# Optimization experiments

Hardware: AMD Instinct MI355X
Metric: run time of the kernel (lower is better)

The kernel has to match this reference:

```python
import jax, jax.numpy as jnp
import numpy as np

B, S, DIM, NQ, NKV = 2, 2048, 4096, 32, 8
HD = DIM // NQ  # 128


def _rope(t, fc):
    # t: [B,S,H,D]; fc: [S,D/2,2] = (cos,sin). Complex multiply on (even,odd) pairs.
    b, s, h, d = t.shape
    tp = t.astype(jnp.float32).reshape(b, s, h, d // 2, 2)
    c = fc[None, :, None, :, 0]
    sn = fc[None, :, None, :, 1]
    x0, x1 = tp[..., 0], tp[..., 1]
    rot = jnp.stack([x0 * c - x1 * sn, x0 * sn + x1 * c], axis=-1)
    return rot.reshape(b, s, h, d).astype(t.dtype)


def setup_inputs() -> dict:
    key = jax.random.key(0)
    ks = jax.random.split(key, 5)
    x = jax.random.normal(ks[0], (B, S, DIM), jnp.float32)
    wq = jax.random.normal(ks[1], (DIM, NQ * HD), jnp.float32) * 0.02
    wk = jax.random.normal(ks[2], (DIM, NKV * HD), jnp.float32) * 0.02
    wv = jax.random.normal(ks[3], (DIM, NKV * HD), jnp.float32) * 0.02
    wo = jax.random.normal(ks[4], (NQ * HD, DIM), jnp.float32) * 0.02
    # Llama RoPE frequencies for positions [0, S)
    inv_freq = 1.0 / (10000.0 ** (jnp.arange(0, HD, 2, dtype=jnp.float32) / HD))
    ang = jnp.arange(S, dtype=jnp.float32)[:, None] * inv_freq[None, :]  # [S, HD/2]
    freqs_cis = jnp.stack([jnp.cos(ang), jnp.sin(ang)], axis=-1)  # [S, HD/2, 2]
    cache_key = jnp.zeros((B, S, NKV, HD), jnp.float32)
    cache_value = jnp.zeros((B, S, NKV, HD), jnp.float32)
    return {"x": x, "start_pos": 0, "freqs_cis": freqs_cis, "wq": wq, "wk": wk,
            "wv": wv, "wo": wo, "cache_key": cache_key, "cache_value": cache_value}


def reference(x, start_pos, freqs_cis, wq, wk, wv, wo, cache_key, cache_value):
    b, s, dim = x.shape
    nkv, hd = cache_key.shape[2], cache_key.shape[3]
    nq = wq.shape[1] // hd
    n_rep = nq // nkv
    xq = (x @ wq).reshape(b, s, nq, hd)
    xk = (x @ wk).reshape(b, s, nkv, hd)
    xv = (x @ wv).reshape(b, s, nkv, hd)
    xq = _rope(xq, freqs_cis)
    xk = _rope(xk, freqs_cis)
    # KV-cache write then read of the valid prefix
    ck = jax.lax.dynamic_update_slice(cache_key, xk, (0, start_pos, 0, 0))
    cv = jax.lax.dynamic_update_slice(cache_value, xv, (0, start_pos, 0, 0))
    kv_len = start_pos + s
    k = ck[:, :kv_len]
    v = cv[:, :kv_len]
    # GQA: repeat_interleave kv heads to match q heads (as original materializes)
    keys = jnp.repeat(k, n_rep, axis=2)    # [B,K,NQ,HD]
    values = jnp.repeat(v, n_rep, axis=2)
    scale = 1.0 / jnp.sqrt(jnp.float32(hd))
    scores = jnp.einsum('bqhd,bkhd->bhqk', xq, keys) * scale  # [B,H,S,K]
    attn = jax.nn.softmax(scores, axis=-1)  # NOTE: no causal mask, as in source
    out = jnp.einsum('bhqk,bkhd->bqhd', attn, values).reshape(b, s, nq * hd)
    return out @ wo
```

## Files before the change

kernel.cpp:

```cpp
#include <hip/hip_runtime.h>
#include <stdint.h>


typedef __attribute__((ext_vector_type(8))) short short8;
typedef __attribute__((ext_vector_type(4))) float f32x4;
typedef __attribute__((ext_vector_type(16))) float f32x16;

#define DEVFN static __device__ __forceinline__

DEVFN ushort f2bf(float f) {
  uint32_t u = __builtin_bit_cast(uint32_t, f);
  u += 0x7fffu + ((u >> 16) & 1);
  return (ushort)(u >> 16);
}

DEVFN void gll16(const void* g, void* l) {
  __builtin_amdgcn_global_load_lds(
      (const __attribute__((address_space(1))) void*)g,
      (__attribute__((address_space(3))) void*)l, 16, 0, 0);
}

DEVFN float xhalf_max(float v) { return fmaxf(v, __shfl_xor(v, 32)); }
DEVFN float xhalf_add(float v) { return v + __shfl_xor(v, 32); }

#if __has_builtin(__builtin_amdgcn_exp2f)
DEVFN float ex2(float x) { return __builtin_amdgcn_exp2f(x); }
#else
DEVFN float ex2(float x) {
  float r;
  asm("v_exp_f32 %0, %1" : "=v"(r) : "v"(x));
  return r;
}
#endif

DEVFN uint32_t cvtpk(float a, float b) {
  uint32_t r;
  asm("v_cvt_pk_bf16_f32 %0, %1, %2" : "=v"(r) : "v"(a), "v"(b));
  return r;
}

DEVFN float vmax16(const f32x16& v) {
  float a0 = fmaxf(fmaxf(v[0], v[1]), v[2]);
  float a1 = fmaxf(fmaxf(v[3], v[4]), v[5]);
  float a2 = fmaxf(fmaxf(v[6], v[7]), v[8]);
  float a3 = fmaxf(fmaxf(v[9], v[10]), v[11]);
  float a4 = fmaxf(fmaxf(v[12], v[13]), v[14]);
  float b0 = fmaxf(fmaxf(a0, a1), a2);
  float b1 = fmaxf(fmaxf(a3, a4), v[15]);
  return fmaxf(b0, b1);
}
DEVFN float vsum16(const f32x16& v) {
  float s0 = (v[0] + v[1]) + (v[2] + v[3]);
  float s1 = (v[4] + v[5]) + (v[6] + v[7]);
  float s2 = (v[8] + v[9]) + (v[10] + v[11]);
  float s3 = (v[12] + v[13]) + (v[14] + v[15]);
  return (s0 + s1) + (s2 + s3);
}

DEVFN short8 mk_frag(uint32_t w0, uint32_t w1, uint32_t w2, uint32_t w3, int hi) {
  uint32_t x0 = __shfl_xor(w0, 32);
  uint32_t x1 = __shfl_xor(w1, 32);
  uint32_t x2 = __shfl_xor(w2, 32);
  uint32_t x3 = __shfl_xor(w3, 32);
  uint4 u;
  u.x = hi ? x2 : w0;
  u.y = hi ? x3 : w1;
  u.z = hi ? w2 : x0;
  u.w = hi ? w3 : x1;
  return __builtin_bit_cast(short8, u);
}

#define VMW(N) asm volatile("s_waitcnt vmcnt(" #N ")" ::: "memory")

__global__ __launch_bounds__(256) void k_cvt(const float* __restrict__ src,
                                             ushort* __restrict__ dst, int n8) {
  int i = blockIdx.x * 256 + threadIdx.x;
  if (i >= n8) return;
  const float4* s4 = (const float4*)src + (size_t)i * 2;
  float4 a = s4[0], b = s4[1];
  uint4 o;
  o.x = (uint32_t)f2bf(a.x) | ((uint32_t)f2bf(a.y) << 16);
  o.y = (uint32_t)f2bf(a.z) | ((uint32_t)f2bf(a.w) << 16);
  o.z = (uint32_t)f2bf(b.x) | ((uint32_t)f2bf(b.y) << 16);
  o.w = (uint32_t)f2bf(b.z) | ((uint32_t)f2bf(b.w) << 16);
  ((uint4*)dst)[i] = o;
}

__global__ __launch_bounds__(256) void k_tr(const float* __restrict__ src,
                                            ushort* __restrict__ dst, int R, int C) {
  __shared__ ushort tl[64 * 64];
  const int c0 = blockIdx.x * 64, r0 = blockIdx.y * 64;
  const int t = threadIdx.x;
  const int r = t >> 4, c4 = (t & 15) << 2;
#pragma unroll
  for (int i = 0; i < 4; ++i) {
    const int rr = r + i * 16;
    float4 v = *(const float4*)&src[(size_t)(r0 + rr) * C + c0 + c4];
    ushort bv[4] = {f2bf(v.x), f2bf(v.y), f2bf(v.z), f2bf(v.w)};
#pragma unroll
    for (int j = 0; j < 4; ++j) {
      const int c = c4 + j;
      *(ushort*)((char*)tl + c * 128 + (((rr >> 3) ^ (c & 7)) << 4) +
                 ((rr & 7) << 1)) = bv[j];
    }
  }
  __syncthreads();
  const int cc = t >> 2;
#pragma unroll
  for (int i = 0; i < 2; ++i) {
    const int ch = (t & 3) + i * 4;
    short8 v = *(const short8*)((char*)tl + cc * 128 + ((ch ^ (cc & 7)) << 4));
    *(short8*)&dst[(size_t)(c0 + cc) * R + r0 + ch * 8] = v;
  }
}

template <int MODE>
__global__ __launch_bounds__(512, 2) void k_gemm8(
    const ushort* __restrict__ A, const ushort* __restrict__ Bp,
    const float* __restrict__ fcis, ushort* __restrict__ oQ,
    ushort* __restrict__ oK, ushort* __restrict__ oV, float* __restrict__ oC) {
  constexpr int K = 4096;
  constexpr int BN = MODE ? 256 : 192;
  constexpr int NBX = MODE ? 16 : 32;
  constexpr int ABUF = 16384;
  constexpr int BBUF = BN * 64;
  constexpr int NT = K / 32;
  constexpr int WNG = MODE ? 4 : 2;
  constexpr int MF = MODE ? 8 : 4;
  constexpr int NF = MODE ? 4 : 6;
  constexpr int MH = MF / 2;
  constexpr int MSPAN = 16 * MF;
  constexpr int NSPAN = 16 * NF;

  __shared__ char smem[4 * ABUF + 4 * BBUF];
  char* AsL = smem;
  char* BsL = smem + 4 * ABUF;

  constexpr int nwg = NBX * 16;
  const int bid = blockIdx.x;
  const int wg = (bid & 7) * (nwg >> 3) + (bid >> 3);
  const int nb = wg % NBX, mb = wg / NBX;
  const int m0 = mb * 256, n0 = nb * BN;

  const int tid = threadIdx.x;
  const int w = tid >> 6, lane = tid & 63;
  const int gg = lane >> 4, rr = lane & 15;
  const int wm = w / WNG, wn = w % WNG;

  const int l8 = lane >> 3, s7 = lane & 7;
  const int Ra0 = w * 8 + l8, Ra1 = 64 + Ra0;
  const int ea0 = s7 ^ (Ra0 & 7), ea1 = s7 ^ (Ra1 & 7);
  const ushort* agp0 = A + (size_t)(m0 + 2 * Ra0 + (ea0 >> 2)) * K + (ea0 & 3) * 8;
  const ushort* agp1 = A + (size_t)(m0 + 2 * Ra1 + (ea1 >> 2)) * K + (ea1 & 3) * 8;
  char* lda0 = AsL + w * 1024;
  char* lda1 = AsL + 8192 + w * 1024;

  const int Rb0 = w * 8 + l8;
  const int eb0 = s7 ^ (Rb0 & 7);
  const ushort* bgp0 = Bp + (size_t)(n0 + 2 * Rb0 + (eb0 >> 2)) * K + (eb0 & 3) * 8;
  char* ldb0 = BsL + w * 1024;
  const int Rb1 = MODE ? (64 + w * 8 + l8) : (64 + w * 4 + l8);
  const int eb1 = s7 ^ (Rb1 & 7);
  const ushort* bgp1 = Bp + (size_t)(n0 + 2 * Rb1 + (eb1 >> 2)) * K + (eb1 & 3) * 8;
  char* ldb1 = BsL + 8192 + (MODE ? w * 1024 : w * 512);

  auto STAGE_A = [&](int t) {
    const int bo = t & 3;
    const size_t ko = (size_t)t * 32;
    gll16(agp0 + ko, lda0 + bo * ABUF);
    gll16(agp1 + ko, lda1 + bo * ABUF);
  };
  auto STAGE_B = [&](int t) {
    const int bo = t & 3;
    const size_t ko = (size_t)t * 32;
    gll16(bgp0 + ko, ldb0 + bo * BBUF);
    if constexpr (MODE) {
      gll16(bgp1 + ko, ldb1 + bo * BBUF);
    } else {
      if (lane < 32) gll16(bgp1 + ko, ldb1 + bo * BBUF);
    }
  };

  int aoff[MF], boff[NF];
#pragma unroll
  for (int mf = 0; mf < MF; ++mf) {
    const int m = wm * MSPAN + mf * 16 + rr;
    aoff[mf] = (m >> 1) * 128 + (((((m & 1) << 2) | gg) ^ ((m >> 1) & 7)) << 4);
  }
#pragma unroll
  for (int nf = 0; nf < NF; ++nf) {
    const int n = wn * NSPAN + nf * 16 + rr;
    boff[nf] = (n >> 1) * 128 + (((((n & 1) << 2) | gg) ^ ((n >> 1) & 7)) << 4);
  }

  f32x4 acc[MF][NF] = {};
  short8 X0[MH], X1[MH], Y0[MH], Y1[MH];
  short8 Bc0[NF], Bc1[NF];

  auto RD_A = [&](int tt, short8* d, int h) {
    const char* Ab = AsL + (tt & 3) * ABUF;
#pragma unroll
    for (int i = 0; i < MH; ++i) d[i] = *(const short8*)(Ab + aoff[h * MH + i]);
  };
  auto RD_B = [&](int tt, short8* d) {
    const char* Bb = BsL + (tt & 3) * BBUF;
#pragma unroll
    for (int nf = 0; nf < NF; ++nf) d[nf] = *(const short8*)(Bb + boff[nf]);
  };
  auto MFMA_H = [&](short8* a, short8* bfr, int h) {
#pragma unroll
    for (int mi = 0; mi < MH; ++mi)
#pragma unroll
      for (int nf = 0; nf < NF; ++nf)
        acc[h + mi][nf] = __builtin_amdgcn_mfma_f32_16x16x32_bf16(
            a[mi], bfr[nf], acc[h + mi][nf], 0, 0, 0);
  };

#define GITER(T, cA0, cA1, cB, nA0, nA1, nB, STG, VN)                \
  do {                                                               \
    if constexpr (MODE == 1) RD_B((T), Bc0); \
    RD_A((T) + 1, nA0, 0);                                           \
    if constexpr (MODE == 0) RD_B((T) + 1, nB);                      \
    __builtin_amdgcn_sched_barrier(0);                               \
    __builtin_amdgcn_s_setprio(1);                                   \
    MFMA_H(cA0, (MODE == 1) ? Bc0 : cB, 0);                          \
    __builtin_amdgcn_s_setprio(0);                                   \
    RD_A((T) + 1, nA1, 1);                                           \
    if (STG) { STAGE_A((T) + 3); STAGE_B((T) + 3); }                 \
    __builtin_amdgcn_sched_barrier(0);                               \
    __builtin_amdgcn_s_setprio(1);                                   \
    MFMA_H(cA1, (MODE == 1) ? Bc0 : cB, MH);                         \
    __builtin_amdgcn_s_setprio(0);                                   \
    VMW(VN);                                                         \
    __builtin_amdgcn_s_barrier();                                    \
    __builtin_amdgcn_sched_barrier(0);                               \
  } while (0)

  STAGE_A(0); STAGE_B(0);
  STAGE_A(1); STAGE_B(1);
  STAGE_A(2); STAGE_B(2);
  VMW(4);
  __builtin_amdgcn_s_barrier();
  __builtin_amdgcn_sched_barrier(0);
  RD_A(0, X0, 0);
  RD_A(0, X1, 1);
  if constexpr (MODE == 0) RD_B(0, Bc0);

  for (int tp = 0; tp < 62; ++tp) {
    const int T = 2 * tp;
    GITER(T, X0, X1, Bc0, Y0, Y1, Bc1, true, 4);
    GITER(T + 1, Y0, Y1, Bc1, X0, X1, Bc0, true, 4);
  }
  GITER(124, X0, X1, Bc0, Y0, Y1, Bc1, true, 4);
  GITER(125, Y0, Y1, Bc1, X0, X1, Bc0, false, 0);
  GITER(126, X0, X1, Bc0, Y0, Y1, Bc1, false, 0);
  if constexpr (MODE == 1) RD_B(127, Bc0);
  __builtin_amdgcn_s_setprio(1);
  MFMA_H(Y0, (MODE == 1) ? Bc0 : Bc1, 0);
  MFMA_H(Y1, (MODE == 1) ? Bc0 : Bc1, MH);
  __builtin_amdgcn_s_setprio(0);
#undef GITER

  if constexpr (MODE == 1) {
#pragma unroll
    for (int mf = 0; mf < MF; ++mf) {
      const int mbase = m0 + wm * MSPAN + mf * 16 + gg * 4;
#pragma unroll
      for (int nf = 0; nf < NF; ++nf) {
        const int n = n0 + wn * NSPAN + nf * 16 + rr;
#pragma unroll
        for (int j = 0; j < 4; ++j)
          oC[(size_t)(mbase + j) * 4096 + n] = acc[mf][nf][j];
      }
    }
  } else {
    const int b = m0 >> 11;
#pragma unroll
    for (int mf = 0; mf < MF; ++mf) {
      const int mbase = m0 + wm * MSPAN + mf * 16 + gg * 4;
      const int s0 = mbase & 2047;
#pragma unroll
      for (int nf = 0; nf < NF; ++nf) {
        const int n = n0 + wn * NSPAN + nf * 16 + rr;
        if (n < 5120) {
          const int d = n & 127, ii = d >> 1;
          const float sgn = (n & 1) ? 1.0f : -1.0f;
          const float qsc = (n < 4096) ? 0.12752364599362f : 1.0f;
          ushort res[4];
#pragma unroll
          for (int j = 0; j < 4; ++j) {
            const float2 cs = ((const float2*)fcis)[(size_t)(s0 + j) * 64 + ii];
            float v = acc[mf][nf][j];
            float pv = __shfl_xor(v, 1);
            res[j] = f2bf(qsc * (v * cs.x + sgn * pv * cs.y));
          }
          if (n < 4096) {
            ushort* dst = oQ + ((size_t)(b * 32 + (n >> 7)) * 2048 + s0) * 128 + d;
#pragma unroll
            for (int j = 0; j < 4; ++j) dst[j * 128] = res[j];
          } else {
            ushort* dst =
                oK + ((size_t)(b * 8 + ((n - 4096) >> 7)) * 2048 + s0) * 128 + d;
#pragma unroll
            for (int j = 0; j < 4; ++j) dst[j * 128] = res[j];
          }
        } else {
          const int n2 = n - 5120;
          ushort4 pk;
          pk.x = f2bf(acc[mf][nf][0]);
          pk.y = f2bf(acc[mf][nf][1]);
          pk.z = f2bf(acc[mf][nf][2]);
          pk.w = f2bf(acc[mf][nf][3]);
          *(ushort4*)&oV[((size_t)(b * 8 + (n2 >> 7)) * 128 + (n2 & 127)) * 2048 + s0] =
              pk;
        }
      }
    }
  }
}

__global__ __launch_bounds__(512, 2) void k_attn(const ushort* __restrict__ Qg,
                                                 const ushort* __restrict__ Kg,
                                                 const ushort* __restrict__ Vt,
                                                 ushort* __restrict__ Og) {
  __shared__ ushort Ks[2][64 * 128];
  __shared__ ushort Vs[2][64 * 128];
  __shared__ float sml[8][32];

  const int bh = blockIdx.x, qt = blockIdx.y;
  const int b = bh >> 5, h = bh & 31, hk = h >> 2;
  const int t = threadIdx.x, w = t >> 6, lane = t & 63;
  const int ln31 = lane & 31, hi = lane >> 5;
  const int q0 = qt * 256;

  short8 qf[8];
  {
    const size_t qbase = ((size_t)bh * 2048 + q0 + w * 32 + ln31) * 128;
#pragma unroll
    for (int tt = 0; tt < 8; ++tt)
      qf[tt] = *(const short8*)&Qg[qbase + tt * 16 + hi * 8];
  }
  const size_t kgb = (size_t)(b * 8 + hk) * 2048 * 128;
  const size_t vgb = (size_t)(b * 8 + hk) * 128 * 2048;

  const int srow = t >> 3;
  const int ssl = (t & 7) * 2;
  const int s0 = ssl ^ (srow & 15);
  const int vd = 2 * (t >> 3) + ((t & 7) >> 2);
  const int vkl = (t & 3) * 16;
  const ushort* kgp = Kg + kgb + (size_t)srow * 128 + ssl * 8;
  const ushort* vgp = Vt + vgb + (size_t)vd * 2048 + vkl;

  uint4 rk0, rk1, rv0, rv1;
  auto LOAD = [&](int k0) {
    const uint4* kp = (const uint4*)(kgp + (size_t)k0 * 128);
    rk0 = kp[0];
    rk1 = kp[1];
    const uint4* vp = (const uint4*)(vgp + k0);
    rv0 = vp[0];
    rv1 = vp[1];
  };
  auto STORE = [&](int buf) {
    char* kd = (char*)Ks[buf] + srow * 256;
    *(uint4*)(kd + (s0 << 4)) = rk0;
    *(uint4*)(kd + ((s0 ^ 1) << 4)) = rk1;
    char* vdd = (char*)Vs[buf] + srow * 256;
    *(uint4*)(vdd + (s0 << 4)) = rv0;
    *(uint4*)(vdd + ((s0 ^ 1) << 4)) = rv1;
  };

  f32x16 ov[4] = {};
  float m_run = -1e30f, l_run = 0.f;

  const int mk = ln31 & 15;
  const int krb0 = ln31 * 256, krb1 = krb0 + 8192;
  const int vrb = (ln31 >> 1) * 256;
  const int vsp = (ln31 & 1) * 8 + hi;
  const int mv = ln31 >> 1;

  LOAD(0);
  STORE(0);
  __syncthreads();

  for (int tile = 0; tile < 32; ++tile) {
    const int cur = tile & 1;
    if (tile < 31) LOAD((tile + 1) * 64);

    const char* Kc = (const char*)Ks[cur];
    f32x16 p0 = {}, p1 = {};
    __builtin_amdgcn_s_setprio(1);
#pragma unroll
    for (int tt = 0; tt < 8; ++tt) {
      const int sl = ((tt * 2 + hi) ^ mk) << 4;
      short8 ka0 = *(const short8*)(Kc + krb0 + sl);
      short8 ka1 = *(const short8*)(Kc + krb1 + sl);
      p0 = __builtin_amdgcn_mfma_f32_32x32x16_bf16(ka0, qf[tt], p0, 0, 0, 0);
      p1 = __builtin_amdgcn_mfma_f32_32x32x16_bf16(ka1, qf[tt], p1, 0, 0, 0);
    }
    __builtin_amdgcn_s_setprio(0);

    const float pmax = xhalf_max(fmaxf(vmax16(p0), vmax16(p1)));
    if (!__all(pmax <= m_run + 8.0f)) {
      const float mnew = fmaxf(m_run, pmax);
      const float al = ex2(m_run - mnew);
      m_run = mnew;
      l_run *= al;
      sml[w][ln31] = al;
      const float4 a0 = *(const float4*)&sml[w][hi * 4];
      const float4 a1 = *(const float4*)&sml[w][8 + hi * 4];
      const float4 a2 = *(const float4*)&sml[w][16 + hi * 4];
      const float4 a3 = *(const float4*)&sml[w][24 + hi * 4];
      const float aa[16] = {a0.x, a0.y, a0.z, a0.w, a1.x, a1.y, a1.z, a1.w,
                            a2.x, a2.y, a2.z, a2.w, a3.x, a3.y, a3.z, a3.w};
#pragma unroll
      for (int i = 0; i < 16; ++i) {
        ov[0][i] *= aa[i]; ov[1][i] *= aa[i];
        ov[2][i] *= aa[i]; ov[3][i] *= aa[i];
      }
    }
#pragma unroll
    for (int i = 0; i < 16; ++i) p0[i] = ex2(p0[i] - m_run);
#pragma unroll
    for (int i = 0; i < 16; ++i) p1[i] = ex2(p1[i] - m_run);
    l_run += xhalf_add(vsum16(p0) + vsum16(p1));

    short8 pa[4];
    pa[0] = mk_frag(cvtpk(p0[0], p0[1]), cvtpk(p0[2], p0[3]),
                    cvtpk(p0[4], p0[5]), cvtpk(p0[6], p0[7]), hi);
    pa[1] = mk_frag(cvtpk(p0[8], p0[9]), cvtpk(p0[10], p0[11]),
                    cvtpk(p0[12], p0[13]), cvtpk(p0[14], p0[15]), hi);
    pa[2] = mk_frag(cvtpk(p1[0], p1[1]), cvtpk(p1[2], p1[3]),
                    cvtpk(p1[4], p1[5]), cvtpk(p1[6], p1[7]), hi);
    pa[3] = mk_frag(cvtpk(p1[8], p1[9]), cvtpk(p1[10], p1[11]),
                    cvtpk(p1[12], p1[13]), cvtpk(p1[14], p1[15]), hi);

    const char* Vc = (const char*)Vs[cur];
    __builtin_amdgcn_s_setprio(1);
#pragma unroll
    for (int db = 0; db < 4; ++db) {
      const int rb = vrb + db * 4096;
#pragma unroll
      for (int ks = 0; ks < 4; ++ks) {
        const int sl = ((vsp + ks * 2) ^ mv) << 4;
        short8 bv = *(const short8*)(Vc + rb + sl);
        ov[db] = __builtin_amdgcn_mfma_f32_32x32x16_bf16(pa[ks], bv, ov[db], 0, 0, 0);
      }
    }
    __builtin_amdgcn_s_setprio(0);

    if (tile < 31) STORE(cur ^ 1);
    __syncthreads();
  }

  sml[w][ln31] = l_run;
  const float4 l0 = *(const float4*)&sml[w][hi * 4];
  const float4 l1 = *(const float4*)&sml[w][8 + hi * 4];
  const float4 l2 = *(const float4*)&sml[w][16 + hi * 4];
  const float4 l3 = *(const float4*)&sml[w][24 + hi * 4];
  const float inv[16] = {1.f / l0.x, 1.f / l0.y, 1.f / l0.z, 1.f / l0.w,
                         1.f / l1.x, 1.f / l1.y, 1.f / l1.z, 1.f / l1.w,
                         1.f / l2.x, 1.f / l2.y, 1.f / l2.z, 1.f / l2.w,
                         1.f / l3.x, 1.f / l3.y, 1.f / l3.z, 1.f / l3.w};
  const int qb0 = q0 + w * 32 + hi * 4;
#pragma unroll
  for (int rg = 0; rg < 4; ++rg)
#pragma unroll
    for (int j = 0; j < 4; ++j) {
      const int sq = qb0 + rg * 8 + j;
      const size_t orow = ((size_t)(b * 2048 + sq)) * 4096 + h * 128 + ln31;
#pragma unroll
      for (int db = 0; db < 4; ++db)
        Og[orow + db * 32] = f2bf(ov[db][rg * 4 + j] * inv[rg * 4 + j]);
    }
}

extern "C" void kernel_launch(void* const* d_in, const int* in_sizes, int n_in,
                              void* d_out, int out_size, void* d_ws, size_t ws_size,
                              hipStream_t stream) {
  const float* x = (const float*)d_in[0];
  const float* fcis = (const float*)d_in[2];
  const float* wq = (const float*)d_in[3];
  const float* wk = (const float*)d_in[4];
  const float* wv = (const float*)d_in[5];
  const float* wo = (const float*)d_in[6];
  float* out = (float*)d_out;

  char* ws = (char*)d_ws;
  ushort* xb  = (ushort*)(ws);
  ushort* wsT = (ushort*)(ws + 33554432u);
  ushort* qb  = (ushort*)(ws + 83886080u);
  ushort* kb  = (ushort*)(ws + 117440512u);
  ushort* vbT = (ushort*)(ws + 125829120u);
  ushort* woT = xb;
  ushort* ao  = wsT;

  k_cvt<<<8192, 256, 0, stream>>>(x, xb, 2097152);
  k_tr<<<dim3(64, 64), 256, 0, stream>>>(wq, wsT, 4096, 4096);
  k_tr<<<dim3(16, 64), 256, 0, stream>>>(wk, wsT + (size_t)4096 * 4096, 4096, 1024);
  k_tr<<<dim3(16, 64), 256, 0, stream>>>(wv, wsT + (size_t)5120 * 4096, 4096, 1024);
  k_gemm8<0><<<512, 512, 0, stream>>>(xb, wsT, fcis, qb, kb, vbT, nullptr);
  k_tr<<<dim3(64, 64), 256, 0, stream>>>(wo, woT, 4096, 4096);
  k_attn<<<dim3(64, 8), 512, 0, stream>>>(qb, kb, vbT, ao);
  k_gemm8<1><<<256, 512, 0, stream>>>(ao, woT, nullptr, nullptr, nullptr, nullptr,
                                      out);
}
```

Measured before the change: 527.7 us.

## Deepen GEMM LDS ring to five stages and barrier every other iteration

The bf16 GEMM's LDS staging ring grows from four to five buffers, with prefetch distance raised from three to four k-tiles. Buffer offsets are tracked with rotating indices instead of `t & 3`. The workgroup barrier plus waits now run only every second k-iteration, and an explicit lgkmcnt(0) is added before each barrier. The goal is more latency hiding and fewer barrier stalls. The cost is about 160 KB of LDS, the full per-CU budget, and a risk of read/write races on buffers reused between barriers.

```diff
diff --git a/kernel.cpp b/kernel.cpp
--- a/kernel.cpp
+++ b/kernel.cpp
@@ -71,6 +71,7 @@
 }
 
 #define VMW(N) asm volatile("s_waitcnt vmcnt(" #N ")" ::: "memory")
+#define LGKM0 asm volatile("s_waitcnt lgkmcnt(0)" ::: "memory")
 
 __global__ __launch_bounds__(256) void k_cvt(const float* __restrict__ src,
                                              ushort* __restrict__ dst, int n8) {
@@ -132,9 +133,9 @@
   constexpr int MSPAN = 16 * MF;
   constexpr int NSPAN = 16 * NF;
 
-  __shared__ char smem[4 * ABUF + 4 * BBUF];
+  __shared__ char smem[5 * ABUF + 5 * BBUF];
   char* AsL = smem;
-  char* BsL = smem + 4 * ABUF;
+  char* BsL = smem + 5 * ABUF;
 
   constexpr int nwg = NBX * 16;
   const int bid = blockIdx.x;
@@ -164,20 +165,18 @@
   const ushort* bgp1 = Bp + (size_t)(n0 + 2 * Rb1 + (eb1 >> 2)) * K + (eb1 & 3) * 8;
   char* ldb1 = BsL + 8192 + (MODE ? w * 1024 : w * 512);
 
-  auto STAGE_A = [&](int t) {
-    const int bo = t & 3;
+  auto STAGE_A = [&](int t, int oo) {
     const size_t ko = (size_t)t * 32;
-    gll16(agp0 + ko, lda0 + bo * ABUF);
-    gll16(agp1 + ko, lda1 + bo * ABUF);
-  };
-  auto STAGE_B = [&](int t) {
-    const int bo = t & 3;
+    gll16(agp0 + ko, lda0 + oo);
+    gll16(agp1 + ko, lda1 + oo);
+  };
+  auto STAGE_B = [&](int t, int oo) {
     const size_t ko = (size_t)t * 32;
-    gll16(bgp0 + ko, ldb0 + bo * BBUF);
+    gll16(bgp0 + ko, ldb0 + oo);
     if constexpr (MODE) {
-      gll16(bgp1 + ko, ldb1 + bo * BBUF);
+      gll16(bgp1 + ko, ldb1 + oo);
     } else {
-      if (lane < 32) gll16(bgp1 + ko, ldb1 + bo * BBUF);
+      if (lane < 32) gll16(bgp1 + ko, ldb1 + oo);
     }
   };
 
@@ -197,13 +196,13 @@
   short8 X0[MH], X1[MH], Y0[MH], Y1[MH];
   short8 Bc0[NF], Bc1[NF];
 
-  auto RD_A = [&](int tt, short8* d, int h) {
-    const char* Ab = AsL + (tt & 3) * ABUF;
+  auto RD_A = [&](int oo, short8* d, int h) {
+    const char* Ab = AsL + oo;
 #pragma unroll
     for (int i = 0; i < MH; ++i) d[i] = *(const short8*)(Ab + aoff[h * MH + i]);
   };
-  auto RD_B = [&](int tt, short8* d) {
-    const char* Bb = BsL + (tt & 3) * BBUF;
+  auto RD_B = [&](int oo, short8* d) {
+    const char* Bb = BsL + oo;
 #pragma unroll
     for (int nf = 0; nf < NF; ++nf) d[nf] = *(const short8*)(Bb + boff[nf]);
   };
@@ -216,45 +215,60 @@
             a[mi], bfr[nf], acc[h + mi][nf], 0, 0, 0);
   };
 
-#define GITER(T, cA0, cA1, cB, nA0, nA1, nB, STG, VN)                \
-  do {                                                               \
-    if constexpr (MODE == 1) RD_B((T), Bc0); \
-    RD_A((T) + 1, nA0, 0);                                           \
-    if constexpr (MODE == 0) RD_B((T) + 1, nB);                      \
-    __builtin_amdgcn_sched_barrier(0);                               \
-    __builtin_amdgcn_s_setprio(1);                                   \
-    MFMA_H(cA0, (MODE == 1) ? Bc0 : cB, 0);                          \
-    __builtin_amdgcn_s_setprio(0);                                   \
-    RD_A((T) + 1, nA1, 1);                                           \
-    if (STG) { STAGE_A((T) + 3); STAGE_B((T) + 3); }                 \
-    __builtin_amdgcn_sched_barrier(0);                               \
-    __builtin_amdgcn_s_setprio(1);                                   \
-    MFMA_H(cA1, (MODE == 1) ? Bc0 : cB, MH);                         \
-    __builtin_amdgcn_s_setprio(0);                                   \
-    VMW(VN);                                                         \
-    __builtin_amdgcn_s_barrier();                                    \
-    __builtin_amdgcn_sched_barrier(0);                               \
+  int oA = 0, oB = 0;
+#define NXTA(o) ((o) + ABUF == 5 * ABUF ? 0 : (o) + ABUF)
+#define NXTB(o) ((o) + BBUF == 5 * BBUF ? 0 : (o) + BBUF)
+#define PRVA(o) ((o) == 0 ? 4 * ABUF : (o)-ABUF)
+#define PRVB(o) ((o) == 0 ? 4 * BBUF : (o)-BBUF)
+
+#define GITER(T, cA0, cA1, cB, nA0, nA1, nB, STG, BARM, VN)           \
+  do {                                                                \
+    const int nAo = NXTA(oA), nBo = NXTB(oB);                         \
+    if constexpr (MODE == 1) RD_B(oB, Bc0);  \
+    RD_A(nAo, nA0, 0);                                                \
+    if constexpr (MODE == 0) RD_B(nBo, nB);                           \
+    __builtin_amdgcn_sched_barrier(0);                                \
+    __builtin_amdgcn_s_setprio(1);                                    \
+    MFMA_H(cA0, (MODE == 1) ? Bc0 : cB, 0);                           \
+    __builtin_amdgcn_s_setprio(0);                                    \
+    RD_A(nAo, nA1, 1);                                                \
+    if (STG) { STAGE_A((T) + 4, PRVA(oA)); STAGE_B((T) + 4, PRVB(oB)); } \
+    __builtin_amdgcn_sched_barrier(0);                                \
+    __builtin_amdgcn_s_setprio(1);                                    \
+    MFMA_H(cA1, (MODE == 1) ? Bc0 : cB, MH);                          \
+    __builtin_amdgcn_s_setprio(0);                                    \
+    if (BARM) {                                                       \
+      LGKM0;                                                          \
+      VMW(VN);                                                        \
+      __builtin_amdgcn_s_barrier();                                   \
+      __builtin_amdgcn_sched_barrier(0);                              \
+    }                                                                 \
+    oA = nAo; oB = nBo;                                               \
   } while (0)
 
-  STAGE_A(0); STAGE_B(0);
-  STAGE_A(1); STAGE_B(1);
-  STAGE_A(2); STAGE_B(2);
+  STAGE_A(0, 0); STAGE_B(0, 0);
+  STAGE_A(1, ABUF); STAGE_B(1, BBUF);
+  STAGE_A(2, 2 * ABUF); STAGE_B(2, 2 * BBUF);
+  STAGE_A(3, 3 * ABUF); STAGE_B(3, 3 * BBUF);
   VMW(4);
   __builtin_amdgcn_s_barrier();
   __builtin_amdgcn_sched_barrier(0);
   RD_A(0, X0, 0);
   RD_A(0, X1, 1);
   if constexpr (MODE == 0) RD_B(0, Bc0);
+  LGKM0;
+  __builtin_amdgcn_s_barrier();
+  __builtin_amdgcn_sched_barrier(0);
 
   for (int tp = 0; tp < 62; ++tp) {
     const int T = 2 * tp;
-    GITER(T, X0, X1, Bc0, Y0, Y1, Bc1, true, 4);
-    GITER(T + 1, Y0, Y1, Bc1, X0, X1, Bc0, true, 4);
-  }
-  GITER(124, X0, X1, Bc0, Y0, Y1, Bc1, true, 4);
-  GITER(125, Y0, Y1, Bc1, X0, X1, Bc0, false, 0);
-  GITER(126, X0, X1, Bc0, Y0, Y1, Bc1, false, 0);
-  if constexpr (MODE == 1) RD_B(127, Bc0);
+    GITER(T, X0, X1, Bc0, Y0, Y1, Bc1, true, 0, 4);
+    GITER(T + 1, Y0, Y1, Bc1, X0, X1, Bc0, true, 1, 4);
+  }
+  GITER(124, X0, X1, Bc0, Y0, Y1, Bc1, false, 0, 4);
+  GITER(125, Y0, Y1, Bc1, X0, X1, Bc0, false, 1, 0);
+  GITER(126, X0, X1, Bc0, Y0, Y1, Bc1, false, 0, 4);
+  if constexpr (MODE == 1) RD_B(oB, Bc0);
   __builtin_amdgcn_s_setprio(1);
   MFMA_H(Y0, (MODE == 1) ? Bc0 : Bc1, 0);
   MFMA_H(Y1, (MODE == 1) ? Bc0 : Bc1, MH);
```

New measurement: 530.5 us. Within noise of the previous version (+0.5%).

## Restructure attention kernel: 64 query rows per wave, triple-buffered direct-to-LDS KV loads

Applied to the files above, without the earlier changes.

Each wave in the attention kernel now handles two 32-row query blocks that share each K and V fragment read from LDS. This halves LDS traffic per MFMA and doubles the query tile per block to 512, which also halves the grid. KV tiles shrink to 32 keys and are streamed with global_load_lds into a three-slot ring. This replaces the register round-trip and store-to-LDS double buffer and allows one barrier per tile. The costs are more accumulator registers, half as many blocks, and twice as many loop iterations.

```diff
diff --git a/kernel.cpp b/kernel.cpp
--- a/kernel.cpp
+++ b/kernel.cpp
@@ -218,7 +218,7 @@
 
 #define GITER(T, cA0, cA1, cB, nA0, nA1, nB, STG, VN)                \
   do {                                                               \
-    if constexpr (MODE == 1) RD_B((T), Bc0); \
+    if constexpr (MODE == 1) RD_B((T), Bc0);                         \
     RD_A((T) + 1, nA0, 0);                                           \
     if constexpr (MODE == 0) RD_B((T) + 1, nB);                      \
     __builtin_amdgcn_sched_barrier(0);                               \
@@ -323,155 +323,179 @@
                                                  const ushort* __restrict__ Kg,
                                                  const ushort* __restrict__ Vt,
                                                  ushort* __restrict__ Og) {
-  __shared__ ushort Ks[2][64 * 128];
-  __shared__ ushort Vs[2][64 * 128];
+  __shared__ ushort Ks[3 * 4096];
+  __shared__ ushort Vs[3 * 4096];
   __shared__ float sml[8][32];
 
   const int bh = blockIdx.x, qt = blockIdx.y;
   const int b = bh >> 5, h = bh & 31, hk = h >> 2;
   const int t = threadIdx.x, w = t >> 6, lane = t & 63;
   const int ln31 = lane & 31, hi = lane >> 5;
-  const int q0 = qt * 256;
-
-  short8 qf[8];
+  const int q0 = qt * 512;
+
+  short8 qfA[8], qfB[8];
   {
-    const size_t qbase = ((size_t)bh * 2048 + q0 + w * 32 + ln31) * 128;
-#pragma unroll
-    for (int tt = 0; tt < 8; ++tt)
-      qf[tt] = *(const short8*)&Qg[qbase + tt * 16 + hi * 8];
-  }
+    const size_t qbase = ((size_t)bh * 2048 + q0 + w * 64 + ln31) * 128;
+#pragma unroll
+    for (int tt = 0; tt < 8; ++tt) {
+      qfA[tt] = *(const short8*)&Qg[qbase + tt * 16 + hi * 8];
+      qfB[tt] = *(const short8*)&Qg[qbase + 32 * 128 + tt * 16 + hi * 8];
+    }
+  }
+
+  const int srow = w * 4 + (lane >> 4);
+  const int ssl = lane & 15;
   const size_t kgb = (size_t)(b * 8 + hk) * 2048 * 128;
   const size_t vgb = (size_t)(b * 8 + hk) * 128 * 2048;
-
-  const int srow = t >> 3;
-  const int ssl = (t & 7) * 2;
-  const int s0 = ssl ^ (srow & 15);
-  const int vd = 2 * (t >> 3) + ((t & 7) >> 2);
-  const int vkl = (t & 3) * 16;
-  const ushort* kgp = Kg + kgb + (size_t)srow * 128 + ssl * 8;
-  const ushort* vgp = Vt + vgb + (size_t)vd * 2048 + vkl;
-
-  uint4 rk0, rk1, rv0, rv1;
-  auto LOAD = [&](int k0) {
-    const uint4* kp = (const uint4*)(kgp + (size_t)k0 * 128);
-    rk0 = kp[0];
-    rk1 = kp[1];
-    const uint4* vp = (const uint4*)(vgp + k0);
-    rv0 = vp[0];
-    rv1 = vp[1];
+  const ushort* kgp = Kg + kgb + (size_t)srow * 128 + ((ssl ^ (srow & 15)) << 3);
+  const int vsi = ssl ^ (srow & 15);
+  const ushort* vgp =
+      Vt + vgb + (size_t)(srow * 4 + (vsi >> 2)) * 2048 + (vsi & 3) * 8;
+  char* kld = (char*)Ks + w * 1024;
+  char* vld = (char*)Vs + w * 1024;
+
+  auto STAGE = [&](int tt) {
+    const int sl = tt - (tt / 3) * 3;
+    gll16(kgp + (size_t)tt * 4096, kld + sl * 8192);
+    gll16(vgp + (size_t)tt * 32, vld + sl * 8192);
   };
-  auto STORE = [&](int buf) {
-    char* kd = (char*)Ks[buf] + srow * 256;
-    *(uint4*)(kd + (s0 << 4)) = rk0;
-    *(uint4*)(kd + ((s0 ^ 1) << 4)) = rk1;
-    char* vdd = (char*)Vs[buf] + srow * 256;
-    *(uint4*)(vdd + (s0 << 4)) = rv0;
-    *(uint4*)(vdd + ((s0 ^ 1) << 4)) = rv1;
-  };
-
-  f32x16 ov[4] = {};
-  float m_run = -1e30f, l_run = 0.f;
+
+  f32x16 ovA[4] = {}, ovB[4] = {};
+  float mA = -1e30f, lA = 0.f, mB = -1e30f, lB = 0.f;
 
   const int mk = ln31 & 15;
-  const int krb0 = ln31 * 256, krb1 = krb0 + 8192;
-  const int vrb = (ln31 >> 1) * 256;
-  const int vsp = (ln31 & 1) * 8 + hi;
-  const int mv = ln31 >> 1;
-
-  LOAD(0);
-  STORE(0);
+  const int krb = ln31 * 256;
+  const int vr0 = ln31 >> 2;
+  const int vsp = (ln31 & 3) * 4 + hi;
+
+  STAGE(0);
+  STAGE(1);
+  VMW(2);
   __syncthreads();
 
-  for (int tile = 0; tile < 32; ++tile) {
-    const int cur = tile & 1;
-    if (tile < 31) LOAD((tile + 1) * 64);
-
-    const char* Kc = (const char*)Ks[cur];
-    f32x16 p0 = {}, p1 = {};
+  for (int tile = 0; tile < 64; ++tile) {
+    const int sl = tile - (tile / 3) * 3;
+    if (tile < 62) STAGE(tile + 2);
+
+    const char* Kc = (const char*)Ks + sl * 8192;
+    f32x16 pA = {}, pB = {};
     __builtin_amdgcn_s_setprio(1);
 #pragma unroll
     for (int tt = 0; tt < 8; ++tt) {
-      const int sl = ((tt * 2 + hi) ^ mk) << 4;
-      short8 ka0 = *(const short8*)(Kc + krb0 + sl);
-      short8 ka1 = *(const short8*)(Kc + krb1 + sl);
-      p0 = __builtin_amdgcn_mfma_f32_32x32x16_bf16(ka0, qf[tt], p0, 0, 0, 0);
-      p1 = __builtin_amdgcn_mfma_f32_32x32x16_bf16(ka1, qf[tt], p1, 0, 0, 0);
+      short8 ka = *(const short8*)(Kc + krb + (((tt * 2 + hi) ^ mk) << 4));
+      pA = __builtin_amdgcn_mfma_f32_32x32x16_bf16(ka, qfA[tt], pA, 0, 0, 0);
+      pB = __builtin_amdgcn_mfma_f32_32x32x16_bf16(ka, qfB[tt], pB, 0, 0, 0);
     }
     __builtin_amdgcn_s_setprio(0);
 
-    const float pmax = xhalf_max(fmaxf(vmax16(p0), vmax16(p1)));
-    if (!__all(pmax <= m_run + 8.0f)) {
-      const float mnew = fmaxf(m_run, pmax);
-      const float al = ex2(m_run - mnew);
-      m_run = mnew;
-      l_run *= al;
-      sml[w][ln31] = al;
-      const float4 a0 = *(const float4*)&sml[w][hi * 4];
-      const float4 a1 = *(const float4*)&sml[w][8 + hi * 4];
-      const float4 a2 = *(const float4*)&sml[w][16 + hi * 4];
-      const float4 a3 = *(const float4*)&sml[w][24 + hi * 4];
-      const float aa[16] = {a0.x, a0.y, a0.z, a0.w, a1.x, a1.y, a1.z, a1.w,
-                            a2.x, a2.y, a2.z, a2.w, a3.x, a3.y, a3.z, a3.w};
-#pragma unroll
-      for (int i = 0; i < 16; ++i) {
-        ov[0][i] *= aa[i]; ov[1][i] *= aa[i];
-        ov[2][i] *= aa[i]; ov[3][i] *= aa[i];
+    short8 paA0, paA1, paB0, paB1;
+    {
+      const float pmax = xhalf_max(vmax16(pA));
+      if (!__all(pmax <= mA + 8.0f)) {
+        const float mnew = fmaxf(mA, pmax);
+        const float al = ex2(mA - mnew);
+        mA = mnew;
+        lA *= al;
+        sml[w][ln31] = al;
+        const float4 a0 = *(const float4*)&sml[w][hi * 4];
+        const float4 a1 = *(const float4*)&sml[w][8 + hi * 4];
+        const float4 a2 = *(const float4*)&sml[w][16 + hi * 4];
+        const float4 a3 = *(const float4*)&sml[w][24 + hi * 4];
+        const float aa[16] = {a0.x, a0.y, a0.z, a0.w, a1.x, a1.y, a1.z, a1.w,
+                              a2.x, a2.y, a2.z, a2.w, a3.x, a3.y, a3.z, a3.w};
+#pragma unroll
+        for (int i = 0; i < 16; ++i) {
+          ovA[0][i] *= aa[i]; ovA[1][i] *= aa[i];
+          ovA[2][i] *= aa[i]; ovA[3][i] *= aa[i];
+        }
       }
-    }
-#pragma unroll
-    for (int i = 0; i < 16; ++i) p0[i] = ex2(p0[i] - m_run);
-#pragma unroll
-    for (int i = 0; i < 16; ++i) p1[i] = ex2(p1[i] - m_run);
-    l_run += xhalf_add(vsum16(p0) + vsum16(p1));
-
-    short8 pa[4];
-    pa[0] = mk_frag(cvtpk(p0[0], p0[1]), cvtpk(p0[2], p0[3]),
-                    cvtpk(p0[4], p0[5]), cvtpk(p0[6], p0[7]), hi);
-    pa[1] = mk_frag(cvtpk(p0[8], p0[9]), cvtpk(p0[10], p0[11]),
-                    cvtpk(p0[12], p0[13]), cvtpk(p0[14], p0[15]), hi);
-    pa[2] = mk_frag(cvtpk(p1[0], p1[1]), cvtpk(p1[2], p1[3]),
-                    cvtpk(p1[4], p1[5]), cvtpk(p1[6], p1[7]), hi);
-    pa[3] = mk_frag(cvtpk(p1[8], p1[9]), cvtpk(p1[10], p1[11]),
-                    cvtpk(p1[12], p1[13]), cvtpk(p1[14], p1[15]), hi);
-
-    const char* Vc = (const char*)Vs[cur];
+#pragma unroll
+      for (int i = 0; i < 16; ++i) pA[i] = ex2(pA[i] - mA);
+      lA += xhalf_add(vsum16(pA));
+      paA0 = mk_frag(cvtpk(pA[0], pA[1]), cvtpk(pA[2], pA[3]),
+                     cvtpk(pA[4], pA[5]), cvtpk(pA[6], pA[7]), hi);
+      paA1 = mk_frag(cvtpk(pA[8], pA[9]), cvtpk(pA[10], pA[11]),
+                     cvtpk(pA[12], pA[13]), cvtpk(pA[14], pA[15]), hi);
+    }
+    {
+      const float pmax = xhalf_max(vmax16(pB));
+      if (!__all(pmax <= mB + 8.0f)) {
+        const float mnew = fmaxf(mB, pmax);
+        const float al = ex2(mB - mnew);
+        mB = mnew;
+        lB *= al;
+        sml[w][ln31] = al;
+        const float4 a0 = *(const float4*)&sml[w][hi * 4];
+        const float4 a1 = *(const float4*)&sml[w][8 + hi * 4];
+        const float4 a2 = *(const float4*)&sml[w][16 + hi * 4];
+        const float4 a3 = *(const float4*)&sml[w][24 + hi * 4];
+        const float aa[16] = {a0.x, a0.y, a0.z, a0.w, a1.x, a1.y, a1.z, a1.w,
+                              a2.x, a2.y, a2.z, a2.w, a3.x, a3.y, a3.z, a3.w};
+#pragma unroll
+        for (int i = 0; i < 16; ++i) {
+          ovB[0][i] *= aa[i]; ovB[1][i] *= aa[i];
+          ovB[2][i] *= aa[i]; ovB[3][i] *= aa[i];
+        }
+      }
+#pragma unroll
+      for (int i = 0; i < 16; ++i) pB[i] = ex2(pB[i] - mB);
+      lB += xhalf_add(vsum16(pB));
+      paB0 = mk_frag(cvtpk(pB[0], pB[1]), cvtpk(pB[2], pB[3]),
+                     cvtpk(pB[4], pB[5]), cvtpk(pB[6], pB[7]), hi);
+      paB1 = mk_frag(cvtpk(pB[8], pB[9]), cvtpk(pB[10], pB[11]),
+                     cvtpk(pB[12], pB[13]), cvtpk(pB[14], pB[15]), hi);
+    }
+
+    const char* Vc = (const char*)Vs + sl * 8192;
     __builtin_amdgcn_s_setprio(1);
 #pragma unroll
     for (int db = 0; db < 4; ++db) {
-      const int rb = vrb + db * 4096;
-#pragma unroll
-      for (int ks = 0; ks < 4; ++ks) {
-        const int sl = ((vsp + ks * 2) ^ mv) << 4;
-        short8 bv = *(const short8*)(Vc + rb + sl);
-        ov[db] = __builtin_amdgcn_mfma_f32_32x32x16_bf16(pa[ks], bv, ov[db], 0, 0, 0);
+      const int row = db * 8 + vr0;
+      const int rb = row * 256;
+      const int rm = row & 15;
+#pragma unroll
+      for (int ks = 0; ks < 2; ++ks) {
+        short8 bv = *(const short8*)(Vc + rb + (((vsp + ks * 2) ^ rm) << 4));
+        const short8 pa_ = ks ? paA1 : paA0;
+        const short8 pb_ = ks ? paB1 : paB0;
+        ovA[db] = __builtin_amdgcn_mfma_f32_32x32x16_bf16(pa_, bv, ovA[db], 0, 0, 0);
+        ovB[db] = __builtin_amdgcn_mfma_f32_32x32x16_bf16(pb_, bv, ovB[db], 0, 0, 0);
       }
     }
     __builtin_amdgcn_s_setprio(0);
 
-    if (tile < 31) STORE(cur ^ 1);
-    __syncthreads();
-  }
-
-  sml[w][ln31] = l_run;
-  const float4 l0 = *(const float4*)&sml[w][hi * 4];
-  const float4 l1 = *(const float4*)&sml[w][8 + hi * 4];
-  const float4 l2 = *(const float4*)&sml[w][16 + hi * 4];
-  const float4 l3 = *(const float4*)&sml[w][24 + hi * 4];
-  const float inv[16] = {1.f / l0.x, 1.f / l0.y, 1.f / l0.z, 1.f / l0.w,
-                         1.f / l1.x, 1.f / l1.y, 1.f / l1.z, 1.f / l1.w,
-                         1.f / l2.x, 1.f / l2.y, 1.f / l2.z, 1.f / l2.w,
-                         1.f / l3.x, 1.f / l3.y, 1.f / l3.z, 1.f / l3.w};
-  const int qb0 = q0 + w * 32 + hi * 4;
-#pragma unroll
-  for (int rg = 0; rg < 4; ++rg)
-#pragma unroll
-    for (int j = 0; j < 4; ++j) {
-      const int sq = qb0 + rg * 8 + j;
-      const size_t orow = ((size_t)(b * 2048 + sq)) * 4096 + h * 128 + ln31;
-#pragma unroll
-      for (int db = 0; db < 4; ++db)
-        Og[orow + db * 32] = f2bf(ov[db][rg * 4 + j] * inv[rg * 4 + j]);
-    }
+    if (tile < 62) VMW(2);
+    else if (tile == 62) VMW(0);
+    if (tile < 63) {
+      __builtin_amdgcn_s_barrier();
+      __builtin_amdgcn_sched_barrier(0);
+    }
+  }
+
+#pragma unroll
+  for (int qb = 0; qb < 2; ++qb) {
+    sml[w][ln31] = qb ? lB : lA;
+    const float4 l0 = *(const float4*)&sml[w][hi * 4];
+    const float4 l1 = *(const float4*)&sml[w][8 + hi * 4];
+    const float4 l2 = *(const float4*)&sml[w][16 + hi * 4];
+    const float4 l3 = *(const float4*)&sml[w][24 + hi * 4];
+    const float inv[16] = {1.f / l0.x, 1.f / l0.y, 1.f / l0.z, 1.f / l0.w,
+                           1.f / l1.x, 1.f / l1.y, 1.f / l1.z, 1.f / l1.w,
+                           1.f / l2.x, 1.f / l2.y, 1.f / l2.z, 1.f / l2.w,
+                           1.f / l3.x, 1.f / l3.y, 1.f / l3.z, 1.f / l3.w};
+    const f32x16* ov = qb ? ovB : ovA;
+    const int qb0 = q0 + w * 64 + qb * 32 + hi * 4;
+#pragma unroll
+    for (int rg = 0; rg < 4; ++rg)
+#pragma unroll
+      for (int j = 0; j < 4; ++j) {
+        const int sq = qb0 + rg * 8 + j;
+        const size_t orow = ((size_t)(b * 2048 + sq)) * 4096 + h * 128 + ln31;
+#pragma unroll
+        for (int db = 0; db < 4; ++db)
+          Og[orow + db * 32] = f2bf(ov[db][rg * 4 + j] * inv[rg * 4 + j]);
+      }
+  }
 }
 
 extern "C" void kernel_launch(void* const* d_in, const int* in_sizes, int n_in,
@@ -500,7 +524,7 @@
   k_tr<<<dim3(16, 64), 256, 0, stream>>>(wv, wsT + (size_t)5120 * 4096, 4096, 1024);
   k_gemm8<0><<<512, 512, 0, stream>>>(xb, wsT, fcis, qb, kb, vbT, nullptr);
   k_tr<<<dim3(64, 64), 256, 0, stream>>>(wo, woT, 4096, 4096);
-  k_attn<<<dim3(64, 8), 512, 0, stream>>>(qb, kb, vbT, ao);
+  k_attn<<<dim3(64, 4), 512, 0, stream>>>(qb, kb, vbT, ao);
   k_gemm8<1><<<256, 512, 0, stream>>>(ao, woT, nullptr, nullptr, nullptr, nullptr,
                                       out);
 }
```

New measurement: 592.3 us. 12.2% more time.
